# Kernel optimization log

Measured on AMD Instinct MI355X. Metric: run time of the kernel, lower is better.

The kernel has to match this reference:

```python
import jax, jax.numpy as jnp
import numpy as np

TAU = 2.0
BN_EPS = 1e-5
HEADS = 8

# spikingjelly-style Heaviside spike with sigmoid surrogate gradient (alpha=4)
@jax.custom_vjp
def spike(x):
    return (x >= 0.0).astype(x.dtype)

def _spike_fwd(x):
    return (x >= 0.0).astype(x.dtype), x

def _spike_bwd(x, g):
    s = jax.nn.sigmoid(4.0 * x)
    return (g * 4.0 * s * (1.0 - s),)

spike.defvjp(_spike_fwd, _spike_bwd)

def lif(x, thresh):
    """Multi-step LIF (tau=2, decay_input=True, hard reset to 0, detach_reset).
    x: (T, ...) input current; returns spikes of the same shape."""
    def step(v, xt):
        v = v + (xt - v) / TAU          # charge
        s = spike(v - thresh)           # fire
        v = v * (1.0 - jax.lax.stop_gradient(s))  # hard reset, detached
        return v, s
    _, s = jax.lax.scan(step, jnp.zeros_like(x[0]), x)
    return s

def bn(x, gamma, beta, mean, var):
    # inference-mode BatchNorm2d over channel axis 2 of (T,B,C,H,W)
    sh = (1, 1, -1, 1, 1)
    scale = gamma / jnp.sqrt(var + BN_EPS)
    return (x - mean.reshape(sh)) * scale.reshape(sh) + beta.reshape(sh)

def setup_inputs() -> dict:
    key = jax.random.key(0)
    T, B, C, H, W = 4, 16, 512, 16, 16
    ks = jax.random.split(key, 24)
    def wmat(k):
        return jax.random.normal(k, (C, C), jnp.float32) * (1.0 / np.sqrt(C))
    def bnp(k):
        k1, k2, k3, k4 = jax.random.split(k, 4)
        return (jax.random.normal(k1, (C,), jnp.float32) * 0.1 + 1.0,
                jax.random.normal(k2, (C,), jnp.float32) * 0.1,
                jax.random.normal(k3, (C,), jnp.float32) * 0.1,
                jax.random.uniform(k4, (C,), jnp.float32) + 0.5)
    qg, qb, qm, qvar = bnp(ks[1]); kg, kb, km, kvar = bnp(ks[3])
    vg, vb, vm, vvar = bnp(ks[5]); pg, pb, pm, pvar = bnp(ks[8])
    return {
        'x': jax.random.normal(ks[0], (T, B, C, H, W), jnp.float32),
        'wq': wmat(ks[10]), 'qg': qg, 'qb': qb, 'qm': qm, 'qvar': qvar,
        'wk': wmat(ks[11]), 'kg': kg, 'kb': kb, 'km': km, 'kvar': kvar,
        'wv': wmat(ks[12]), 'vg': vg, 'vb': vb, 'vm': vm, 'vvar': vvar,
        'wp': wmat(ks[13]), 'bp': jax.random.normal(ks[14], (C,), jnp.float32) * 0.02,
        'pg': pg, 'pb': pb, 'pm': pm, 'pvar': pvar,
    }

def reference(x, wq, qg, qb, qm, qvar, wk, kg, kb, km, kvar,
              wv, vg, vb, vm, vvar, wp, bp, pg, pb, pm, pvar):
    T, B, C, H, W = x.shape
    dh = C // HEADS
    N = H * W
    identity = x
    xs = lif(x, 1.0)  # shortcut_lif

    def branch(w, g, b, m, v):
        y = jnp.einsum('tbchw,oc->tbohw', xs, w)  # 1x1 conv, no bias
        return lif(bn(y, g, b, m, v), 1.0)

    # (T,B,C,H,W) spikes -> (T,B,heads,N,dh)
    def to_heads(s):
        return s.reshape(T, B, HEADS, dh, N).transpose(0, 1, 2, 4, 3)

    q = to_heads(branch(wq, qg, qb, qm, qvar))
    k = to_heads(branch(wk, kg, kb, km, kvar))
    v = to_heads(branch(wv, vg, vb, vm, vvar))

    kv = (k * v).sum(axis=3, keepdims=True)   # sum over tokens N -> (T,B,h,1,dh)
    kv = lif(kv, 0.5)                          # talking_heads_lif (v_threshold=0.5)

    out = q * kv                               # (T,B,h,N,dh)
    out = out.transpose(0, 1, 2, 4, 3).reshape(T, B, C, H, W)
    out = jnp.einsum('tbchw,oc->tbohw', out, wp) + bp.reshape(1, 1, -1, 1, 1)
    out = bn(out, pg, pb, pm, pvar) + identity
    return out, v
```

## Files before the change

kernel.cpp:

```cpp
#include <hip/hip_runtime.h>
#include <hip/hip_bf16.h>

typedef unsigned short u16;
typedef unsigned int u32;
typedef __attribute__((ext_vector_type(8))) short bh8;
typedef __attribute__((ext_vector_type(4))) short sh4;
typedef __attribute__((ext_vector_type(4))) float f4;

#define T_   4
#define B_   16
#define C_   512
#define N_   256
#define M2_  4096

__device__ __forceinline__ u16 f2bf(float f) {
  u32 u = __float_as_uint(f);
  u32 r = (u + 0x7FFFu + ((u >> 16) & 1u)) >> 16;
  return (u16)r;
}
__device__ __forceinline__ void gl_lds16(const void* g, void* l) {
  __builtin_amdgcn_global_load_lds(
      (const __attribute__((address_space(1))) unsigned int*)g,
      (__attribute__((address_space(3))) unsigned int*)l, 16, 0, 0);
}

__global__ void k_prep_lif(const float* __restrict__ x, u16* __restrict__ xs,
                           const float* __restrict__ wq, const float* __restrict__ wk,
                           const float* __restrict__ wv, const float* __restrict__ wp,
                           const float* qg, const float* qb, const float* qm, const float* qv,
                           const float* kg, const float* kb, const float* km, const float* kv2,
                           const float* vg, const float* vb, const float* vm, const float* vv,
                           const float* pg, const float* pb, const float* pm, const float* pv,
                           const float* bp,
                           u16* __restrict__ wcat, u16* __restrict__ wpcat,
                           float* bns, float* pss) {
  __shared__ u16 sp[4][64][68];
  int bid = blockIdx.x;
  int tid = threadIdx.x;
  if (bid < 512) {
    int b = bid >> 5, c0 = ((bid >> 2) & 7) * 64, n0 = (bid & 3) * 64;
    int rq = tid >> 4;
    int n4 = (tid & 15) * 4;
    float v[16];
#pragma unroll
    for (int i = 0; i < 16; i++) v[i] = 0.f;
    for (int t = 0; t < 4; t++) {
      const float* xb = x + (((size_t)t * 16 + b) * 512 + c0) * 256 + n0;
#pragma unroll
      for (int i = 0; i < 4; i++) {
        int row = rq + i * 16;
        f4 xv = *(const f4*)(xb + (size_t)row * 256 + n4);
        sh4 sv;
#pragma unroll
        for (int j = 0; j < 4; j++) {
          float vv2 = v[i * 4 + j];
          vv2 = vv2 + (xv[j] - vv2) * 0.5f;
          u16 s = 0;
          if (vv2 >= 1.0f) { s = 0x3F80; vv2 = 0.f; }
          v[i * 4 + j] = vv2;
          sv[j] = (short)s;
        }
        *(sh4*)&sp[t][row][n4] = sv;
      }
    }
    __syncthreads();
    int cp = (tid & 31) * 2;
    int nq = tid >> 5;
    for (int t = 0; t < 4; t++) {
      u16* ob = xs + (((size_t)t * 16 + b) * 256 + n0) * 512 + c0;
#pragma unroll
      for (int i = 0; i < 8; i++) {
        int n = nq + i * 8;
        u32 w = (u32)sp[t][cp][n] | ((u32)sp[t][cp + 1][n] << 16);
        *(u32*)(ob + (size_t)n * 512 + cp) = w;
      }
    }
  } else {
    int id = (bid - 512) * 256 + tid;
    if (id < 1048576) {
      int mat = id >> 18;
      int rc  = id & 262143;
      int o = rc >> 9, c = rc & 511;
      const float* src = (mat == 0) ? wq : (mat == 1) ? wk : (mat == 2) ? wv : wp;
      float w = src[rc];
      u16 hu = f2bf(w);
      float hf = __uint_as_float(((u32)hu) << 16);
      u16 lu = f2bf(w - hf);
      if (mat < 3) {
        size_t base = ((size_t)(mat * 512 + o)) * 1024 + c;
        wcat[base] = hu; wcat[base + 512] = lu;
      } else {
        size_t base = (size_t)o * 1024 + c;
        wpcat[base] = hu; wpcat[base + 512] = lu;
      }
    } else {
      int j = id - 1048576;
      if (j < 1536) {
        int br = j >> 9, c = j & 511;
        const float *g, *b, *m, *va;
        if (br == 0)      { g = qg; b = qb; m = qm; va = qv; }
        else if (br == 1) { g = kg; b = kb; m = km; va = kv2; }
        else              { g = vg; b = vb; m = vm; va = vv; }
        float s = g[c] / sqrtf(va[c] + 1e-5f);
        bns[j * 4 + 0] = s; bns[j * 4 + 1] = m[c]; bns[j * 4 + 2] = b[c];
        bns[j * 4 + 3] = 0.f;
      } else if (j < 2048) {
        int c = j - 1536;
        float s = pg[c] / sqrtf(pv[c] + 1e-5f);
        pss[c * 4 + 0] = bp[c]; pss[c * 4 + 1] = pm[c];
        pss[c * 4 + 2] = s;     pss[c * 4 + 3] = pb[c];
      }
    }
  }
}

__launch_bounds__(256, 2)
__global__ void k_qkv_gemm(const u16* __restrict__ xs, const u16* __restrict__ wcat,
                           const float* __restrict__ bns,
                           u16* __restrict__ qs, u16* __restrict__ kvsp) {
  __shared__ char lds[81920];
  int tid = threadIdx.x, lane = tid & 63, wid = tid >> 6;
  int wr = wid >> 1, wc = wid & 1, lr = lane & 15, lq = lane >> 4;
  int m0 = blockIdx.x * 128, o0 = blockIdx.y * 96;

  float scl[3], mn[3], bt[3];
#pragma unroll
  for (int ni = 0; ni < 3; ni++) {
    int ch = o0 + wc * 48 + ni * 16 + lr;
    scl[ni] = bns[ch * 4]; mn[ni] = bns[ch * 4 + 1]; bt[ni] = bns[ch * 4 + 2];
  }

  int srow = tid >> 3;
  u32 sgoff = (u32)(((tid & 7) ^ (srow & 7)) << 4);
  u32 ldst = (u32)tid * 16;

  u32 aoff[4], boff[3];
#pragma unroll
  for (int mi = 0; mi < 4; mi++) {
    int r = wr * 64 + mi * 16 + lr;
    aoff[mi] = r * 128 + ((lq ^ (r & 7)) << 4);
  }
#pragma unroll
  for (int ni = 0; ni < 3; ni++) {
    int r = wc * 48 + ni * 16 + lr;
    boff[ni] = r * 128 + ((lq ^ (r & 7)) << 4);
  }

  const char* Bb = (const char*)wcat + (size_t)o0 * 2048;

  auto STAGE = [&](int buf, int step) {
    int t = step >> 3;
    u32 kb = (u32)(step & 7) * 128;
    const char* Ab = (const char*)xs + ((size_t)t * M2_ + m0) * 1024;
    char* L = lds + buf * 40960;
#pragma unroll
    for (int r2 = 0; r2 < 4; r2++)
      gl_lds16(Ab + (size_t)(r2 * 32 + srow) * 1024 + kb + sgoff, L + r2 * 4096 + ldst);
#pragma unroll
    for (int r2 = 0; r2 < 3; r2++) {
      gl_lds16(Bb + (size_t)(r2 * 32 + srow) * 2048 + kb + sgoff, L + 16384 + r2 * 4096 + ldst);
      gl_lds16(Bb + (size_t)(r2 * 32 + srow) * 2048 + 1024 + kb + sgoff, L + 28672 + r2 * 4096 + ldst);
    }
  };

  float vst[4][3][4];
#pragma unroll
  for (int a = 0; a < 4; a++)
#pragma unroll
    for (int b = 0; b < 3; b++)
#pragma unroll
      for (int c = 0; c < 4; c++) vst[a][b][c] = 0.f;

  f4 acc[4][3];
  STAGE(0, 0);
  __syncthreads();
  int cur = 0;
  for (int step = 0; step < 32; ++step) {
    int ks = step & 7;
    if (ks == 0) {
#pragma unroll
      for (int a = 0; a < 4; a++)
#pragma unroll
        for (int b = 0; b < 3; b++) { acc[a][b][0] = 0.f; acc[a][b][1] = 0.f; acc[a][b][2] = 0.f; acc[a][b][3] = 0.f; }
    }
    if (step < 31) STAGE(cur ^ 1, step + 1);
    const char* L = lds + cur * 40960;
#pragma unroll
    for (int h = 0; h < 2; h++) {
      u32 hx = (u32)h << 6;
      bh8 af[4], bf[3], lf[3];
#pragma unroll
      for (int mi = 0; mi < 4; mi++)
        af[mi] = *(const bh8*)(L + (aoff[mi] ^ hx));
#pragma unroll
      for (int ni = 0; ni < 3; ni++) {
        bf[ni] = *(const bh8*)(L + 16384 + (boff[ni] ^ hx));
        lf[ni] = *(const bh8*)(L + 28672 + (boff[ni] ^ hx));
      }
#pragma unroll
      for (int mi = 0; mi < 4; mi++)
#pragma unroll
        for (int ni = 0; ni < 3; ni++)
          acc[mi][ni] = __builtin_amdgcn_mfma_f32_16x16x32_bf16(af[mi], bf[ni], acc[mi][ni], 0, 0, 0);
#pragma unroll
      for (int mi = 0; mi < 4; mi++)
#pragma unroll
        for (int ni = 0; ni < 3; ni++)
          acc[mi][ni] = __builtin_amdgcn_mfma_f32_16x16x32_bf16(af[mi], lf[ni], acc[mi][ni], 0, 0, 0);
    }
    asm volatile("s_waitcnt vmcnt(0)" ::: "memory");
    __builtin_amdgcn_s_barrier();
    cur ^= 1;
    if (ks == 7) {
      int t = step >> 3;
#pragma unroll
      for (int mi = 0; mi < 4; mi++)
#pragma unroll
        for (int ni = 0; ni < 3; ni++)
#pragma unroll
          for (int j = 0; j < 4; j++) {
            float y = acc[mi][ni][j];
            y = (y - mn[ni]) * scl[ni] + bt[ni];
            float vv = vst[mi][ni][j];
            vv = vv + (y - vv) * 0.5f;
            u16 s = 0;
            if (vv >= 1.0f) { s = 0x3F80; vv = 0.f; }
            vst[mi][ni][j] = vv;
            int rg = m0 + wr * 64 + mi * 16 + lq * 4 + j;
            int o = o0 + wc * 48 + ni * 16 + lr;
            size_t rowg = (size_t)t * M2_ + rg;
            if (o < 512) qs[rowg * 512 + o] = s;
            else         kvsp[rowg * 1024 + (o - 512)] = s;
          }
    }
  }
}

__global__ void k_kvv(const u16* __restrict__ kvsp, float* __restrict__ vout,
                      int* __restrict__ kvp) {
  int tb = blockIdx.x >> 3, nc = blockIdx.x & 7;
  int tid = threadIdx.x;
  const char* base = (const char*)kvsp + ((size_t)tb * 256 + nc * 32) * 2048;
  int c = tid * 2, h = c >> 6, d = c & 63;
  float* vo = vout + (((size_t)tb * 8 + h) * 256 + nc * 32) * 64 + d;
  int cnt0 = 0, cnt1 = 0;
  for (int n = 0; n < 32; n++) {
    u32 kk = *(const u32*)(base + (size_t)n * 2048 + c * 2);
    u32 vv = *(const u32*)(base + (size_t)n * 2048 + 1024 + c * 2);
    u32 a = kk & vv;
    cnt0 += (a & 0xFFFFu) ? 1 : 0;
    cnt1 += (a >> 16) ? 1 : 0;
    float2 w;
    w.x = (vv & 0xFFFFu) ? 1.f : 0.f;
    w.y = (vv >> 16) ? 1.f : 0.f;
    *(float2*)(vo + (size_t)n * 64) = w;
  }
  kvp[((tb * 8 + nc) << 9) + c]     = cnt0;
  kvp[((tb * 8 + nc) << 9) + c + 1] = cnt1;
}

__global__ void k_tlif(const int* __restrict__ kvp, unsigned char* __restrict__ mask) {
  int id = blockIdx.x * 256 + threadIdx.x;
  int b = id >> 9, c = id & 511;
  float v = 0.f;
  for (int t = 0; t < 4; t++) {
    int tb = t * 16 + b;
    int s = 0;
#pragma unroll
    for (int nc = 0; nc < 8; nc++) s += kvp[((tb * 8 + nc) << 9) + c];
    float xx = (float)s;
    v = v + (xx - v) * 0.5f;
    unsigned char sp = 0;
    if (v >= 0.5f) { sp = 1; v = 0.f; }
    mask[tb * 512 + c] = sp;
  }
}

__launch_bounds__(256, 2)
__global__ void k_proj_gemm(const u16* __restrict__ qs, const unsigned char* __restrict__ mask,
                            const u16* __restrict__ wpc, const float* __restrict__ pss,
                            const float* __restrict__ x, float* __restrict__ out) {
  __shared__ char lds[66560];
  u16* lm = (u16*)(lds + 65536);
  int tid = threadIdx.x, lane = tid & 63, wid = tid >> 6;
  int wr = wid >> 1, wc = wid & 1, lr = lane & 15, lq = lane >> 4;
  int m0 = blockIdx.x * 128, o0 = blockIdx.y * 64;
  int tb = m0 >> 8;

  lm[tid]       = mask[tb * 512 + tid]       ? (u16)0xFFFF : (u16)0;
  lm[tid + 256] = mask[tb * 512 + tid + 256] ? (u16)0xFFFF : (u16)0;

  int srow = tid >> 3;
  u32 sgoff = (u32)(((tid & 7) ^ (srow & 7)) << 4);
  u32 ldst = (u32)tid * 16;

  u32 aoff[4], boff[2];
#pragma unroll
  for (int mi = 0; mi < 4; mi++) {
    int r = wr * 64 + mi * 16 + lr;
    aoff[mi] = r * 128 + ((lq ^ (r & 7)) << 4);
  }
#pragma unroll
  for (int ni = 0; ni < 2; ni++) {
    int r = wc * 32 + ni * 16 + lr;
    boff[ni] = r * 128 + ((lq ^ (r & 7)) << 4);
  }

  const char* Ab = (const char*)qs + (size_t)m0 * 1024;
  const char* Bb = (const char*)wpc + (size_t)o0 * 2048;

  auto STAGE = [&](int buf, int step) {
    u32 kb = (u32)step * 128;
    char* L = lds + buf * 32768;
#pragma unroll
    for (int r2 = 0; r2 < 4; r2++)
      gl_lds16(Ab + (size_t)(r2 * 32 + srow) * 1024 + kb + sgoff, L + r2 * 4096 + ldst);
#pragma unroll
    for (int r2 = 0; r2 < 2; r2++) {
      gl_lds16(Bb + (size_t)(r2 * 32 + srow) * 2048 + kb + sgoff, L + 16384 + r2 * 4096 + ldst);
      gl_lds16(Bb + (size_t)(r2 * 32 + srow) * 2048 + 1024 + kb + sgoff, L + 24576 + r2 * 4096 + ldst);
    }
  };

  f4 acc[4][2];
#pragma unroll
  for (int a = 0; a < 4; a++)
#pragma unroll
    for (int b = 0; b < 2; b++) { acc[a][b][0] = 0.f; acc[a][b][1] = 0.f; acc[a][b][2] = 0.f; acc[a][b][3] = 0.f; }

  STAGE(0, 0);
  __syncthreads();
  int cur = 0;
  for (int step = 0; step < 8; ++step) {
    u32 kb = (u32)step * 128;
    if (step < 7) STAGE(cur ^ 1, step + 1);
    const char* L = lds + cur * 32768;
#pragma unroll
    for (int h = 0; h < 2; h++) {
      u32 hx = (u32)h << 6;
      bh8 mq = *(const bh8*)((const char*)lm + kb + (h << 6) + lq * 16);
      bh8 af[4], bf[2], lf[2];
#pragma unroll
      for (int mi = 0; mi < 4; mi++) {
        af[mi] = *(const bh8*)(L + (aoff[mi] ^ hx));
        af[mi] = af[mi] & mq;
      }
#pragma unroll
      for (int ni = 0; ni < 2; ni++) {
        bf[ni] = *(const bh8*)(L + 16384 + (boff[ni] ^ hx));
        lf[ni] = *(const bh8*)(L + 24576 + (boff[ni] ^ hx));
      }
#pragma unroll
      for (int mi = 0; mi < 4; mi++)
#pragma unroll
        for (int ni = 0; ni < 2; ni++)
          acc[mi][ni] = __builtin_amdgcn_mfma_f32_16x16x32_bf16(af[mi], bf[ni], acc[mi][ni], 0, 0, 0);
#pragma unroll
      for (int mi = 0; mi < 4; mi++)
#pragma unroll
        for (int ni = 0; ni < 2; ni++)
          acc[mi][ni] = __builtin_amdgcn_mfma_f32_16x16x32_bf16(af[mi], lf[ni], acc[mi][ni], 0, 0, 0);
    }
    asm volatile("s_waitcnt vmcnt(0)" ::: "memory");
    __builtin_amdgcn_s_barrier();
    cur ^= 1;
  }
#pragma unroll
  for (int mi = 0; mi < 4; mi++)
#pragma unroll
    for (int ni = 0; ni < 2; ni++) {
      int o = o0 + wc * 32 + ni * 16 + lr;
      f4 ps = *(const f4*)&pss[o * 4];
      int n = (m0 & 255) + wr * 64 + mi * 16 + lq * 4;
      size_t idx = (size_t)tb * 131072 + (size_t)o * 256 + n;
      f4 xv = *(const f4*)&x[idx];
      f4 res;
#pragma unroll
      for (int j = 0; j < 4; j++) {
        float u = acc[mi][ni][j] + ps[0];
        u = (u - ps[1]) * ps[2] + ps[3];
        res[j] = u + xv[j];
      }
      *(f4*)&out[idx] = res;
    }
}

extern "C" void kernel_launch(void* const* d_in, const int* in_sizes, int n_in,
                              void* d_out, int out_size, void* d_ws, size_t ws_size,
                              hipStream_t stream) {
  const float* x  = (const float*)d_in[0];
  const float* wq = (const float*)d_in[1];
  const float* qg = (const float*)d_in[2];
  const float* qb = (const float*)d_in[3];
  const float* qm = (const float*)d_in[4];
  const float* qv = (const float*)d_in[5];
  const float* wk = (const float*)d_in[6];
  const float* kg = (const float*)d_in[7];
  const float* kb = (const float*)d_in[8];
  const float* km = (const float*)d_in[9];
  const float* kv = (const float*)d_in[10];
  const float* wv = (const float*)d_in[11];
  const float* vg = (const float*)d_in[12];
  const float* vb = (const float*)d_in[13];
  const float* vm = (const float*)d_in[14];
  const float* vv = (const float*)d_in[15];
  const float* wp = (const float*)d_in[16];
  const float* bp = (const float*)d_in[17];
  const float* pg = (const float*)d_in[18];
  const float* pb = (const float*)d_in[19];
  const float* pm = (const float*)d_in[20];
  const float* pv = (const float*)d_in[21];

  char* w = (char*)d_ws;
  u16*  XS    = (u16*)(w + 0);
  u16*  QS    = (u16*)(w + 16777216);
  u16*  KVSP  = (u16*)(w + 33554432);
  u16*  WCAT  = (u16*)(w + 67108864);
  u16*  WPCAT = (u16*)(w + 70254592);
  float* BNS  = (float*)(w + 71303168);
  float* PSS  = (float*)(w + 71327744);
  int*   KVP  = (int*)(w + 71335936);
  unsigned char* MASK = (unsigned char*)(w + 72384512);

  float* out  = (float*)d_out;
  float* vout = out + 8388608;

  k_prep_lif<<<4616, 256, 0, stream>>>(x, XS, wq, wk, wv, wp,
                                       qg, qb, qm, qv, kg, kb, km, kv,
                                       vg, vb, vm, vv, pg, pb, pm, pv, bp,
                                       WCAT, WPCAT, BNS, PSS);
  k_qkv_gemm<<<dim3(32, 16), 256, 0, stream>>>(XS, WCAT, BNS, QS, KVSP);
  k_kvv<<<512, 256, 0, stream>>>(KVSP, vout, KVP);
  k_tlif<<<32, 256, 0, stream>>>(KVP, MASK);
  k_proj_gemm<<<dim3(128, 8), 256, 0, stream>>>(QS, MASK, WPCAT, PSS, x, out);
}
```

Measured before the change: 213.7 us.

## Triple-buffer QKV GEMM, swizzle block order, vectorize kvv and prep loads

The QKV GEMM moves from double to triple LDS buffering, prefetching two stages ahead with partial vmcnt waits and a barrier at the top of each step, so global loads overlap MFMA work more deeply. Both GEMMs remap block IDs in an XCD-aware order, intended to improve L2 locality across the chiplets. The kvv kernel now reads 16-byte vectors and writes float4 outputs and int4 counts, and the prep kernel issues all four timestep loads before running the LIF recurrence. In exchange, the larger LDS footprint (120KB) likely cuts the QKV GEMM occupancy to one block per CU, and the extra barrier adds sync cost.

```diff
diff --git a/kernel.cpp b/kernel.cpp
--- a/kernel.cpp
+++ b/kernel.cpp
@@ -41,20 +41,27 @@
     int b = bid >> 5, c0 = ((bid >> 2) & 7) * 64, n0 = (bid & 3) * 64;
     int rq = tid >> 4;
     int n4 = (tid & 15) * 4;
-    float v[16];
-#pragma unroll
-    for (int i = 0; i < 16; i++) v[i] = 0.f;
+    f4 xr[4][4];
+#pragma unroll
     for (int t = 0; t < 4; t++) {
       const float* xb = x + (((size_t)t * 16 + b) * 512 + c0) * 256 + n0;
 #pragma unroll
+      for (int i = 0; i < 4; i++)
+        xr[t][i] = *(const f4*)(xb + (size_t)(rq + i * 16) * 256 + n4);
+    }
+    float v[16];
+#pragma unroll
+    for (int i = 0; i < 16; i++) v[i] = 0.f;
+#pragma unroll
+    for (int t = 0; t < 4; t++) {
+#pragma unroll
       for (int i = 0; i < 4; i++) {
         int row = rq + i * 16;
-        f4 xv = *(const f4*)(xb + (size_t)row * 256 + n4);
         sh4 sv;
 #pragma unroll
         for (int j = 0; j < 4; j++) {
           float vv2 = v[i * 4 + j];
-          vv2 = vv2 + (xv[j] - vv2) * 0.5f;
+          vv2 = vv2 + (xr[t][i][j] - vv2) * 0.5f;
           u16 s = 0;
           if (vv2 >= 1.0f) { s = 0x3F80; vv2 = 0.f; }
           v[i * 4 + j] = vv2;
@@ -118,10 +125,12 @@
 __global__ void k_qkv_gemm(const u16* __restrict__ xs, const u16* __restrict__ wcat,
                            const float* __restrict__ bns,
                            u16* __restrict__ qs, u16* __restrict__ kvsp) {
-  __shared__ char lds[81920];
+  __shared__ char lds[122880];
   int tid = threadIdx.x, lane = tid & 63, wid = tid >> 6;
   int wr = wid >> 1, wc = wid & 1, lr = lane & 15, lq = lane >> 4;
-  int m0 = blockIdx.x * 128, o0 = blockIdx.y * 96;
+  int id = blockIdx.y * 32 + blockIdx.x;
+  int sw = (id & 7) * 64 + (id >> 3);
+  int m0 = (sw & 31) * 128, o0 = (sw >> 5) * 96;
 
   float scl[3], mn[3], bt[3];
 #pragma unroll
@@ -173,17 +182,21 @@
 
   f4 acc[4][3];
   STAGE(0, 0);
-  __syncthreads();
-  int cur = 0;
+  STAGE(1, 1);
   for (int step = 0; step < 32; ++step) {
     int ks = step & 7;
+    int cur = step % 3;
     if (ks == 0) {
 #pragma unroll
       for (int a = 0; a < 4; a++)
 #pragma unroll
         for (int b = 0; b < 3; b++) { acc[a][b][0] = 0.f; acc[a][b][1] = 0.f; acc[a][b][2] = 0.f; acc[a][b][3] = 0.f; }
     }
-    if (step < 31) STAGE(cur ^ 1, step + 1);
+    if (step < 30) STAGE((step + 2) % 3, step + 2);
+    if (step < 30)      asm volatile("s_waitcnt vmcnt(20)" ::: "memory");
+    else if (step == 30) asm volatile("s_waitcnt vmcnt(10)" ::: "memory");
+    else                 asm volatile("s_waitcnt vmcnt(0)" ::: "memory");
+    __builtin_amdgcn_s_barrier();
     const char* L = lds + cur * 40960;
 #pragma unroll
     for (int h = 0; h < 2; h++) {
@@ -208,9 +221,6 @@
         for (int ni = 0; ni < 3; ni++)
           acc[mi][ni] = __builtin_amdgcn_mfma_f32_16x16x32_bf16(af[mi], lf[ni], acc[mi][ni], 0, 0, 0);
     }
-    asm volatile("s_waitcnt vmcnt(0)" ::: "memory");
-    __builtin_amdgcn_s_barrier();
-    cur ^= 1;
     if (ks == 7) {
       int t = step >> 3;
 #pragma unroll
@@ -233,6 +243,7 @@
             else         kvsp[rowg * 1024 + (o - 512)] = s;
           }
     }
+    __builtin_amdgcn_s_barrier();
   }
 }
 
@@ -240,23 +251,37 @@
                       int* __restrict__ kvp) {
   int tb = blockIdx.x >> 3, nc = blockIdx.x & 7;
   int tid = threadIdx.x;
+  int cg = tid & 63;
+  int ns = tid >> 6;
   const char* base = (const char*)kvsp + ((size_t)tb * 256 + nc * 32) * 2048;
-  int c = tid * 2, h = c >> 6, d = c & 63;
-  float* vo = vout + (((size_t)tb * 8 + h) * 256 + nc * 32) * 64 + d;
-  int cnt0 = 0, cnt1 = 0;
-  for (int n = 0; n < 32; n++) {
-    u32 kk = *(const u32*)(base + (size_t)n * 2048 + c * 2);
-    u32 vv = *(const u32*)(base + (size_t)n * 2048 + 1024 + c * 2);
-    u32 a = kk & vv;
-    cnt0 += (a & 0xFFFFu) ? 1 : 0;
-    cnt1 += (a >> 16) ? 1 : 0;
-    float2 w;
-    w.x = (vv & 0xFFFFu) ? 1.f : 0.f;
-    w.y = (vv >> 16) ? 1.f : 0.f;
-    *(float2*)(vo + (size_t)n * 64) = w;
-  }
-  kvp[((tb * 8 + nc) << 9) + c]     = cnt0;
-  kvp[((tb * 8 + nc) << 9) + c + 1] = cnt1;
+  int h = cg >> 3, dd = (cg & 7) * 8;
+  float* vo = vout + ((size_t)tb * 8 + h) * 16384 + (size_t)(nc * 32) * 64 + dd;
+  int cnt[8];
+#pragma unroll
+  for (int j = 0; j < 8; j++) cnt[j] = 0;
+#pragma unroll
+  for (int i = 0; i < 8; i++) {
+    int n = ns + i * 4;
+    uint4 kk = *(const uint4*)(base + (size_t)n * 2048 + cg * 16);
+    uint4 vv = *(const uint4*)(base + (size_t)n * 2048 + 1024 + cg * 16);
+    u32 a0 = kk.x & vv.x, a1 = kk.y & vv.y, a2 = kk.z & vv.z, a3 = kk.w & vv.w;
+    cnt[0] += (a0 & 0xFFFFu) ? 1 : 0; cnt[1] += (a0 >> 16) ? 1 : 0;
+    cnt[2] += (a1 & 0xFFFFu) ? 1 : 0; cnt[3] += (a1 >> 16) ? 1 : 0;
+    cnt[4] += (a2 & 0xFFFFu) ? 1 : 0; cnt[5] += (a2 >> 16) ? 1 : 0;
+    cnt[6] += (a3 & 0xFFFFu) ? 1 : 0; cnt[7] += (a3 >> 16) ? 1 : 0;
+    float4 f0, f1;
+    f0.x = (vv.x & 0xFFFFu) ? 1.f : 0.f; f0.y = (vv.x >> 16) ? 1.f : 0.f;
+    f0.z = (vv.y & 0xFFFFu) ? 1.f : 0.f; f0.w = (vv.y >> 16) ? 1.f : 0.f;
+    f1.x = (vv.z & 0xFFFFu) ? 1.f : 0.f; f1.y = (vv.z >> 16) ? 1.f : 0.f;
+    f1.z = (vv.w & 0xFFFFu) ? 1.f : 0.f; f1.w = (vv.w >> 16) ? 1.f : 0.f;
+    *(float4*)(vo + (size_t)n * 64)     = f0;
+    *(float4*)(vo + (size_t)n * 64 + 4) = f1;
+  }
+  int* kp2 = kvp + (((tb * 8 + nc) << 9) + cg * 8);
+  int4 c0; c0.x = cnt[0]; c0.y = cnt[1]; c0.z = cnt[2]; c0.w = cnt[3];
+  int4 c1; c1.x = cnt[4]; c1.y = cnt[5]; c1.z = cnt[6]; c1.w = cnt[7];
+  *(int4*)kp2 = c0;
+  *(int4*)(kp2 + 4) = c1;
 }
 
 __global__ void k_tlif(const int* __restrict__ kvp, unsigned char* __restrict__ mask) {
@@ -284,7 +309,9 @@
   u16* lm = (u16*)(lds + 65536);
   int tid = threadIdx.x, lane = tid & 63, wid = tid >> 6;
   int wr = wid >> 1, wc = wid & 1, lr = lane & 15, lq = lane >> 4;
-  int m0 = blockIdx.x * 128, o0 = blockIdx.y * 64;
+  int id = blockIdx.y * 128 + blockIdx.x;
+  int sw = (id & 7) * 128 + (id >> 3);
+  int m0 = (sw & 127) * 128, o0 = (sw >> 7) * 64;
   int tb = m0 >> 8;
 
   lm[tid]       = mask[tb * 512 + tid]       ? (u16)0xFFFF : (u16)0;
```

After: 264.4 us. 23.8% more time.
